# Optimization experiments

Measured on AMD Instinct MI355X. Metric: run time of the kernel, lower is better.

## Reference

```python
import jax, jax.numpy as jnp
import numpy as np

GRID_NUM = 7
IMG_SIZE = 448.0
LAMBDA_COORD = 5.0
LAMBDA_NOOBJ = 0.5
NUM_CLASSES = 20
EPS = 1e-12


def setup_inputs() -> dict:
    key = jax.random.key(0)
    k1, k2, k3 = jax.random.split(key, 3)
    B, S = 16384, GRID_NUM
    # predictions in [0,1) so sqrt(w+eps) is valid (module assumes sigmoid-ed outputs)
    y_pre = jax.random.uniform(k1, (B, S, S, 30), dtype=jnp.float32)
    # targets: channel 0 = class_id in {0..20} (0 => no object), 1:5 = (cx,cy,w,h) in [0,1)
    class_id = jax.random.randint(k2, (B, S, S, 1), 0, NUM_CLASSES + 1).astype(jnp.float32)
    rest = jax.random.uniform(k3, (B, S, S, 7), dtype=jnp.float32)
    y_true = jnp.concatenate([class_id, rest], axis=-1)
    return {"y_pre": y_pre, "y_true": y_true}


def _iou(box_pre, box_true, grid_size):
    # box layout: (cx, cy, w, h); cx,cy relative to the grid cell, w,h relative to the image.
    # Both boxes share the same cell offset, so the offset cancels in all corner differences.
    cx1 = box_pre[..., 0] * grid_size
    cy1 = box_pre[..., 1] * grid_size
    w1 = box_pre[..., 2] * IMG_SIZE
    h1 = box_pre[..., 3] * IMG_SIZE
    cx2 = box_true[..., 0] * grid_size
    cy2 = box_true[..., 1] * grid_size
    w2 = box_true[..., 2] * IMG_SIZE
    h2 = box_true[..., 3] * IMG_SIZE
    ix = jnp.maximum(jnp.minimum(cx1 + w1 / 2, cx2 + w2 / 2)
                     - jnp.maximum(cx1 - w1 / 2, cx2 - w2 / 2), 0.0)
    iy = jnp.maximum(jnp.minimum(cy1 + h1 / 2, cy2 + h2 / 2)
                     - jnp.maximum(cy1 - h1 / 2, cy2 - h2 / 2), 0.0)
    inter = ix * iy
    union = w1 * h1 + w2 * h2 - inter
    return inter / (union + EPS)


def reference(y_pre, y_true):
    B = y_pre.shape[0]
    grid_size = IMG_SIZE / GRID_NUM

    obj = y_true[..., 0] != 0.0                      # [B,S,S] cells with an object
    noobj = jnp.logical_not(obj)
    gt_box = y_true[..., 1:5]                        # (cx,cy,w,h)

    iou0 = _iou(y_pre[..., 0:4], gt_box, grid_size)  # [B,S,S]
    iou1 = _iou(y_pre[..., 5:9], gt_box, grid_size)
    choose0 = iou0 > iou1                            # strict > picks box 0, ties -> box 1

    conf_pre = jnp.where(choose0, y_pre[..., 4], y_pre[..., 9])
    conf_true = jnp.where(choose0, iou0, iou1)       # differentiable through y_pre, as in torch

    # confidence loss: responsible box in obj cells, both boxes in no-obj cells
    loss_conf = jnp.sum(jnp.where(obj, (conf_pre - conf_true) ** 2, 0.0))
    loss_conf += LAMBDA_NOOBJ * jnp.sum(
        jnp.where(noobj, y_pre[..., 4] ** 2 + y_pre[..., 9] ** 2, 0.0))

    c0 = choose0[..., None]
    xy_pre = jnp.where(c0, y_pre[..., 0:2], y_pre[..., 5:7])
    wh_pre = jnp.where(c0, y_pre[..., 2:4], y_pre[..., 7:9])

    loss_coord = LAMBDA_COORD * jnp.sum(
        jnp.where(obj, jnp.sum((xy_pre - gt_box[..., 0:2]) ** 2, axis=-1), 0.0))
    loss_scale = LAMBDA_COORD * jnp.sum(
        jnp.where(obj, jnp.sum((jnp.sqrt(wh_pre + EPS)
                                - jnp.sqrt(gt_box[..., 2:4] + EPS)) ** 2, axis=-1), 0.0))

    # class loss: one-hot at class_id-1 (class_id=0 cells are masked out by obj)
    cls_true = jax.nn.one_hot(y_true[..., 0].astype(jnp.int32) - 1,
                              NUM_CLASSES, dtype=y_pre.dtype)
    loss_cls = jnp.sum(jnp.where(
        obj, jnp.sum((y_pre[..., 10:] - cls_true) ** 2, axis=-1), 0.0))

    return (loss_conf + loss_coord + loss_scale + loss_cls) / B
```

## Files before the change

kernel.cpp:

```cpp
#include <hip/hip_runtime.h>

#define GRID_NUM 7
#define IMG_SIZE 448.0f
#define LAMBDA_COORD 5.0f
#define LAMBDA_NOOBJ 0.5f
#define NUM_CLASSES 20
#define YOLO_EPS 1e-12f

#define TPB 256
#define WPB 4

__device__ __forceinline__ float iou_pair(float px, float py, float pw, float ph,
                                          float tx, float ty, float tw, float th) {
    const float gs = IMG_SIZE / (float)GRID_NUM;
    float cx1 = px * gs, cy1 = py * gs, w1 = pw * IMG_SIZE, h1 = ph * IMG_SIZE;
    float cx2 = tx * gs, cy2 = ty * gs, w2 = tw * IMG_SIZE, h2 = th * IMG_SIZE;
    float ix = fmaxf(fminf(cx1 + 0.5f * w1, cx2 + 0.5f * w2) -
                     fmaxf(cx1 - 0.5f * w1, cx2 - 0.5f * w2), 0.0f);
    float iy = fmaxf(fminf(cy1 + 0.5f * h1, cy2 + 0.5f * h2) -
                     fmaxf(cy1 - 0.5f * h1, cy2 - 0.5f * h2), 0.0f);
    float inter = ix * iy;
    float uni = w1 * h1 + w2 * h2 - inter;
    return inter / (uni + YOLO_EPS);
}

__device__ __forceinline__ float cell_loss(const float* __restrict__ p,
                                           float cls, float gx, float gy,
                                           float gw, float gh) {
    bool obj = (cls != 0.0f);
    float iou0 = iou_pair(p[0], p[1], p[2], p[3], gx, gy, gw, gh);
    float iou1 = iou_pair(p[5], p[6], p[7], p[8], gx, gy, gw, gh);
    bool c0 = iou0 > iou1;

    float l = 0.0f;
    if (obj) {
        float conf_pre  = c0 ? p[4] : p[9];
        float conf_true = c0 ? iou0 : iou1;
        float dc = conf_pre - conf_true;
        l += dc * dc;
        float xp = c0 ? p[0] : p[5];
        float yp = c0 ? p[1] : p[6];
        float dx = xp - gx, dy = yp - gy;
        l += LAMBDA_COORD * (dx * dx + dy * dy);
        float wp = c0 ? p[2] : p[7];
        float hp = c0 ? p[3] : p[8];
        float sw = sqrtf(wp + YOLO_EPS) - sqrtf(gw + YOLO_EPS);
        float sh = sqrtf(hp + YOLO_EPS) - sqrtf(gh + YOLO_EPS);
        l += LAMBDA_COORD * (sw * sw + sh * sh);
        int ci = (int)cls - 1;
#pragma unroll
        for (int c = 0; c < NUM_CLASSES; ++c) {
            float tt = (c == ci) ? 1.0f : 0.0f;
            float dd = p[10 + c] - tt;
            l += dd * dd;
        }
    } else {
        l += LAMBDA_NOOBJ * (p[4] * p[4] + p[9] * p[9]);
    }
    return l;
}

__global__ void __launch_bounds__(TPB) yolo_main(
        const float* __restrict__ y_pre, const float* __restrict__ y_true,
        float* __restrict__ partial) {
    __shared__ __align__(16) float sp[WPB][1920];
    __shared__ float wsum[WPB];

    const int t = threadIdx.x;
    const int lane = t & 63;
    const int w = t >> 6;
    const size_t waveCell = (size_t)blockIdx.x * TPB + (size_t)w * 64;

    const float4* gsrc = reinterpret_cast<const float4*>(y_pre + waveCell * 30);
    float* lbase = sp[w];
#pragma unroll
    for (int i = 0; i < 7; ++i) {
        __builtin_amdgcn_global_load_lds(
            (const __attribute__((address_space(1))) void*)(gsrc + i * 64 + lane),
            (__attribute__((address_space(3))) void*)(lbase + i * 256),
            16, 0, 0);
    }
    if (lane < 32) {
        __builtin_amdgcn_global_load_lds(
            (const __attribute__((address_space(1))) void*)(gsrc + 448 + lane),
            (__attribute__((address_space(3))) void*)(lbase + 1792),
            16, 0, 0);
    }

    const float4* tq = reinterpret_cast<const float4*>(y_true + waveCell * 8);
    float4 r0 = tq[lane];
    float4 r1 = tq[64 + lane];

    asm volatile("s_waitcnt vmcnt(0)" ::: "memory");

    const int sl  = (2 * lane) & 63;
    const int slh = (2 * lane + 1) & 63;
    const bool lo = (lane < 32);
    float c0v = __shfl(r0.x, sl, 64),  c1v = __shfl(r1.x, sl, 64);
    float x0v = __shfl(r0.y, sl, 64),  x1v = __shfl(r1.y, sl, 64);
    float y0v = __shfl(r0.z, sl, 64),  y1v = __shfl(r1.z, sl, 64);
    float w0v = __shfl(r0.w, sl, 64),  w1v = __shfl(r1.w, sl, 64);
    float h0v = __shfl(r0.x, slh, 64), h1v = __shfl(r1.x, slh, 64);
    float cls = lo ? c0v : c1v;
    float gx  = lo ? x0v : x1v;
    float gy  = lo ? y0v : y1v;
    float gw  = lo ? w0v : w1v;
    float gh  = lo ? h0v : h1v;

    float p[30];
    const float2* pl = reinterpret_cast<const float2*>(lbase + lane * 30);
#pragma unroll
    for (int i = 0; i < 15; ++i) {
        float2 v = pl[i];
        p[2 * i]     = v.x;
        p[2 * i + 1] = v.y;
    }

    float acc = cell_loss(p, cls, gx, gy, gw, gh);

#pragma unroll
    for (int off = 32; off > 0; off >>= 1)
        acc += __shfl_down(acc, off, 64);

    if (lane == 0) wsum[w] = acc;
    __syncthreads();
    if (t == 0)
        partial[blockIdx.x] = wsum[0] + wsum[1] + wsum[2] + wsum[3];
}

__global__ void __launch_bounds__(256) yolo_reduce(
        const float* __restrict__ partial, float* __restrict__ out,
        int n4, float inv_b) {
    const float4* p4 = reinterpret_cast<const float4*>(partial);
    const int i = threadIdx.x;
    float4 a = p4[i];
    float4 b = p4[i + 256];
    float4 c = p4[i + 512];
    float4 d = (i + 768 < n4) ? p4[i + 768] : make_float4(0.f, 0.f, 0.f, 0.f);

    float s = (a.x + a.y + a.z + a.w) + (b.x + b.y + b.z + b.w) +
              (c.x + c.y + c.z + c.w) + (d.x + d.y + d.z + d.w);

#pragma unroll
    for (int off = 32; off > 0; off >>= 1)
        s += __shfl_down(s, off, 64);

    __shared__ float wsum[4];
    int lane = threadIdx.x & 63, wid = threadIdx.x >> 6;
    if (lane == 0) wsum[wid] = s;
    __syncthreads();
    if (threadIdx.x == 0)
        out[0] = (wsum[0] + wsum[1] + wsum[2] + wsum[3]) * inv_b;
}

extern "C" void kernel_launch(void* const* d_in, const int* in_sizes, int n_in,
                              void* d_out, int out_size, void* d_ws, size_t ws_size,
                              hipStream_t stream) {
    const float* y_pre  = (const float*)d_in[0];
    const float* y_true = (const float*)d_in[1];
    float* out = (float*)d_out;
    float* partial = (float*)d_ws;

    const int B = in_sizes[0] / (GRID_NUM * GRID_NUM * 30);
    const int ncells = B * GRID_NUM * GRID_NUM;
    const float inv_b = 1.0f / (float)B;

    const int grid = ncells / TPB;
    yolo_main<<<grid, TPB, 0, stream>>>(y_pre, y_true, partial);
    yolo_reduce<<<1, 256, 0, stream>>>(partial, out, grid / 4, inv_b);
}
```

Measured before the change: 25.64 us.

## Compute class loss in registers from coalesced loads, stage only box fields in LDS

Replaces the direct global-to-LDS copy of all 30 channels per cell with coalesced float4 register loads. Each lane computes the class-loss terms directly from the elements it loaded, using a small per-wave LDS table of class indices. Only the 10 box/confidence channels are scattered into LDS, at a padded stride of 11, to cut LDS footprint and bank conflicts. The launch bound now asks for 8 blocks per CU, trading more index arithmetic and LDS scatter stores for higher occupancy.

```diff
diff --git a/kernel.cpp b/kernel.cpp
--- a/kernel.cpp
+++ b/kernel.cpp
@@ -9,6 +9,9 @@
 
 #define TPB 256
 #define WPB 4
+#define BOX_STRIDE 11
+#define CITAB_OFF  704
+#define WAVE_WORDS 768
 
 __device__ __forceinline__ float iou_pair(float px, float py, float pw, float ph,
                                           float tx, float ty, float tw, float th) {
@@ -24,46 +27,10 @@
     return inter / (uni + YOLO_EPS);
 }
 
-__device__ __forceinline__ float cell_loss(const float* __restrict__ p,
-                                           float cls, float gx, float gy,
-                                           float gw, float gh) {
-    bool obj = (cls != 0.0f);
-    float iou0 = iou_pair(p[0], p[1], p[2], p[3], gx, gy, gw, gh);
-    float iou1 = iou_pair(p[5], p[6], p[7], p[8], gx, gy, gw, gh);
-    bool c0 = iou0 > iou1;
-
-    float l = 0.0f;
-    if (obj) {
-        float conf_pre  = c0 ? p[4] : p[9];
-        float conf_true = c0 ? iou0 : iou1;
-        float dc = conf_pre - conf_true;
-        l += dc * dc;
-        float xp = c0 ? p[0] : p[5];
-        float yp = c0 ? p[1] : p[6];
-        float dx = xp - gx, dy = yp - gy;
-        l += LAMBDA_COORD * (dx * dx + dy * dy);
-        float wp = c0 ? p[2] : p[7];
-        float hp = c0 ? p[3] : p[8];
-        float sw = sqrtf(wp + YOLO_EPS) - sqrtf(gw + YOLO_EPS);
-        float sh = sqrtf(hp + YOLO_EPS) - sqrtf(gh + YOLO_EPS);
-        l += LAMBDA_COORD * (sw * sw + sh * sh);
-        int ci = (int)cls - 1;
-#pragma unroll
-        for (int c = 0; c < NUM_CLASSES; ++c) {
-            float tt = (c == ci) ? 1.0f : 0.0f;
-            float dd = p[10 + c] - tt;
-            l += dd * dd;
-        }
-    } else {
-        l += LAMBDA_NOOBJ * (p[4] * p[4] + p[9] * p[9]);
-    }
-    return l;
-}
-
-__global__ void __launch_bounds__(TPB) yolo_main(
+__global__ void __launch_bounds__(TPB, 8) yolo_main(
         const float* __restrict__ y_pre, const float* __restrict__ y_true,
         float* __restrict__ partial) {
-    __shared__ __align__(16) float sp[WPB][1920];
+    __shared__ __align__(16) float sp[WPB * WAVE_WORDS];
     __shared__ float wsum[WPB];
 
     const int t = threadIdx.x;
@@ -71,27 +38,18 @@
     const int w = t >> 6;
     const size_t waveCell = (size_t)blockIdx.x * TPB + (size_t)w * 64;
 
-    const float4* gsrc = reinterpret_cast<const float4*>(y_pre + waveCell * 30);
-    float* lbase = sp[w];
-#pragma unroll
-    for (int i = 0; i < 7; ++i) {
-        __builtin_amdgcn_global_load_lds(
-            (const __attribute__((address_space(1))) void*)(gsrc + i * 64 + lane),
-            (__attribute__((address_space(3))) void*)(lbase + i * 256),
-            16, 0, 0);
-    }
-    if (lane < 32) {
-        __builtin_amdgcn_global_load_lds(
-            (const __attribute__((address_space(1))) void*)(gsrc + 448 + lane),
-            (__attribute__((address_space(3))) void*)(lbase + 1792),
-            16, 0, 0);
-    }
+    float* box = sp + w * WAVE_WORDS;
+    int* citab = (int*)(sp + w * WAVE_WORDS + CITAB_OFF);
 
     const float4* tq = reinterpret_cast<const float4*>(y_true + waveCell * 8);
     float4 r0 = tq[lane];
     float4 r1 = tq[64 + lane];
 
-    asm volatile("s_waitcnt vmcnt(0)" ::: "memory");
+    const float4* gp4 = reinterpret_cast<const float4*>(y_pre + waveCell * 30);
+    float4 q0 = gp4[0 * 64 + lane];
+    float4 q1 = gp4[1 * 64 + lane];
+    float4 q2 = gp4[2 * 64 + lane];
+    float4 q3 = gp4[3 * 64 + lane];
 
     const int sl  = (2 * lane) & 63;
     const int slh = (2 * lane + 1) & 63;
@@ -107,16 +65,77 @@
     float gw  = lo ? w0v : w1v;
     float gh  = lo ? h0v : h1v;
 
-    float p[30];
-    const float2* pl = reinterpret_cast<const float2*>(lbase + lane * 30);
+    const bool obj = (cls != 0.0f);
+    const int ci = (int)cls - 1;
+    citab[lane] = obj ? ci : -1;
+
+    float4 q4 = gp4[4 * 64 + lane];
+    float4 q5 = gp4[5 * 64 + lane];
+    float4 q6 = gp4[6 * 64 + lane];
+    float4 q7 = make_float4(0.f, 0.f, 0.f, 0.f);
+    if (lane < 32) q7 = gp4[448 + lane];
+
+    float accc = 0.0f;
+
+    auto proc = [&](float4 v, int fbase, bool act) {
+        int c0 = (fbase * 2185) >> 16;
+        int ch0 = fbase - 30 * c0;
+        float vv0 = v.x, vv1 = v.y, vv2 = v.z, vv3 = v.w;
+        float vs[4] = {vv0, vv1, vv2, vv3};
 #pragma unroll
-    for (int i = 0; i < 15; ++i) {
-        float2 v = pl[i];
-        p[2 * i]     = v.x;
-        p[2 * i + 1] = v.y;
+        for (int e = 0; e < 4; ++e) {
+            int ch = ch0 + e;
+            int c = c0;
+            if (ch >= 30) { ch -= 30; c += 1; }
+            int cic = citab[c];
+            if (ch < 10) {
+                if (act) box[c * BOX_STRIDE + ch] = vs[e];
+            } else {
+                float tt = ((ch - 10) == cic) ? 1.0f : 0.0f;
+                float d = vs[e] - tt;
+                accc += (act && cic >= 0) ? d * d : 0.0f;
+            }
+        }
+    };
+
+    proc(q0, 0 * 256 + 4 * lane, true);
+    proc(q1, 1 * 256 + 4 * lane, true);
+    proc(q2, 2 * 256 + 4 * lane, true);
+    proc(q3, 3 * 256 + 4 * lane, true);
+    proc(q4, 4 * 256 + 4 * lane, true);
+    proc(q5, 5 * 256 + 4 * lane, true);
+    proc(q6, 6 * 256 + 4 * lane, true);
+    proc(q7, 1792 + 4 * (lane & 31), lane < 32);
+
+    float p[10];
+#pragma unroll
+    for (int j = 0; j < 10; ++j) p[j] = box[lane * BOX_STRIDE + j];
+
+    float l = 0.0f;
+    {
+        float iou0 = iou_pair(p[0], p[1], p[2], p[3], gx, gy, gw, gh);
+        float iou1 = iou_pair(p[5], p[6], p[7], p[8], gx, gy, gw, gh);
+        bool ch0b = iou0 > iou1;
+        if (obj) {
+            float conf_pre  = ch0b ? p[4] : p[9];
+            float conf_true = ch0b ? iou0 : iou1;
+            float dc = conf_pre - conf_true;
+            l += dc * dc;
+            float xp = ch0b ? p[0] : p[5];
+            float yp = ch0b ? p[1] : p[6];
+            float dx = xp - gx, dy = yp - gy;
+            l += LAMBDA_COORD * (dx * dx + dy * dy);
+            float wp = ch0b ? p[2] : p[7];
+            float hp = ch0b ? p[3] : p[8];
+            float sw = sqrtf(wp + YOLO_EPS) - sqrtf(gw + YOLO_EPS);
+            float sh = sqrtf(hp + YOLO_EPS) - sqrtf(gh + YOLO_EPS);
+            l += LAMBDA_COORD * (sw * sw + sh * sh);
+        } else {
+            l += LAMBDA_NOOBJ * (p[4] * p[4] + p[9] * p[9]);
+        }
     }
 
-    float acc = cell_loss(p, cls, gx, gy, gw, gh);
+    float acc = accc + l;
 
 #pragma unroll
     for (int off = 32; off > 0; off >>= 1)
```

Result: slower. 30.34 us (+18.3%).
